# Performance work log

Hardware: AMD Instinct MI355X
Metric: run time of the kernel (lower is better)

Reference implementation:

```python
import jax, jax.numpy as jnp
import numpy as np

N = 65536      # points per cloud
L = 64         # voxel grid side
K_KNN = 16


def _decode(lin):
    x = lin // (L * L); y = (lin // L) % L; z = lin % L
    return np.stack([x, y, z], -1).astype(np.int32)


def _build_nbr(out_c, in_c, r):
    # Minkowski-style kernel map: for each output coord and each of (2r+1)^3
    # offsets, index of matching input coord, sentinel=len(in_c) if absent.
    g = np.arange(-r, r + 1)
    offs = np.stack(np.meshgrid(g, g, g, indexing='ij'), -1).reshape(-1, 3)
    S = 80  # encode side (coords in [-r, L+r) shifted by 8 fit in [0,80))
    def enc(c):
        return ((c[..., 0].astype(np.int64) + 8) * S + (c[..., 1] + 8)) * S + (c[..., 2] + 8)
    kin = enc(in_c)
    order = np.argsort(kin).astype(np.int32)
    skin = kin[order]
    nin = len(in_c)
    rows = []
    for i in range(0, len(out_c), 8192):
        q = out_c[i:i + 8192, None, :] + offs[None]
        kq = enc(q).reshape(-1)
        pos = np.clip(np.searchsorted(skin, kq), 0, nin - 1)
        ok = skin[pos] == kq
        rows.append(np.where(ok, order[pos], nin).astype(np.int32).reshape(-1, len(offs)))
    return np.concatenate(rows, 0)


def _knn(qc, rc, k):
    # brute-force knn (matches pytorch3d.ops.knn_points indices up to order;
    # downstream mean/softmax are permutation invariant)
    q = qc.astype(np.float32); r = rc.astype(np.float32)
    rn = (r * r).sum(1)
    out = []
    for i in range(0, len(q), 4096):
        qb = q[i:i + 4096]
        d = (qb * qb).sum(1)[:, None] + rn[None, :] - 2.0 * qb @ r.T
        out.append(np.argpartition(d, k, axis=1)[:, :k].astype(np.int32))
    return np.concatenate(out, 0)


def setup_inputs():
    rng = np.random.default_rng(0)
    prev_C = _decode(rng.permutation(L ** 3)[:N])
    cur_C = _decode(rng.permutation(L ** 3)[:N])
    nbr_interp = _build_nbr(cur_C, prev_C, 4)  # 9^3 = 729 offsets
    nbr3 = _build_nbr(cur_C, cur_C, 1)         # 3^3 = 27 offsets
    knn_idx = _knn(cur_C, prev_C, K_KNN)
    key = jax.random.key(0)
    ks = jax.random.split(key, 32)
    f32 = jnp.float32
    def w(k, shape, s):
        return jax.random.normal(k, shape, f32) * s
    C = 32
    return dict(
        prev_F=w(ks[0], (N, 1), 1.0),
        prev_C=jnp.asarray(prev_C), cur_C=jnp.asarray(cur_C),
        nbr_interp=jnp.asarray(nbr_interp), nbr3=jnp.asarray(nbr3),
        knn_idx=jnp.asarray(knn_idx),
        W_interp=w(ks[1], (729, 1, 1), 0.05), b_interp=w(ks[2], (1,), 0.05),
        W_conv0=w(ks[3], (27, 2, C), 0.1), b_conv0=w(ks[4], (C,), 0.05),
        W_conv1=w(ks[5], (C, C), 0.1), b_conv1=w(ks[6], (C,), 0.05),
        Wi00=w(ks[7], (C, C // 4), 0.1), bi00=w(ks[8], (C // 4,), 0.05),
        Wi01=w(ks[9], (27, C // 4, C // 4), 0.1), bi01=w(ks[10], (C // 4,), 0.05),
        Wi02=w(ks[11], (C // 4, C // 2), 0.1), bi02=w(ks[12], (C // 2,), 0.05),
        Wi10=w(ks[13], (27, C, C // 4), 0.1), bi10=w(ks[14], (C // 4,), 0.05),
        Wi11=w(ks[15], (27, C // 4, C // 2), 0.1), bi11=w(ks[16], (C // 2,), 0.05),
        Wq=w(ks[17], (1, 1), 0.5), bq=w(ks[18], (1,), 0.1),
        Wk=w(ks[19], (4, 1), 0.5), bk=w(ks[20], (1,), 0.1),
        Wv=w(ks[21], (4, 1), 0.5), bv=w(ks[22], (1,), 0.1),
        Wlin=w(ks[23], (1, 1), 0.5), blin=w(ks[24], (1,), 0.1),
        ln1_g=jnp.ones((1,), f32), ln1_b=jnp.zeros((1,), f32),
        ln2_g=jnp.ones((1,), f32), ln2_b=jnp.zeros((1,), f32),
    )


def _sparse_conv(feats, nbr, W, b):
    # gather-GEMM-scatter sparse conv; sentinel index == len(feats) -> zero row
    fpad = jnp.concatenate([feats, jnp.zeros((1, feats.shape[1]), feats.dtype)], 0)
    g = fpad[nbr]  # [Nout, K, Cin]
    return jnp.einsum('nkc,kcd->nd', g, W) + b


def _ln(x, g, b, eps=1e-5):
    m = jnp.mean(x, -1, keepdims=True)
    v = jnp.var(x, -1, keepdims=True)
    return (x - m) * jax.lax.rsqrt(v + eps) * g + b


def reference(prev_F, prev_C, cur_C, nbr_interp, nbr3, knn_idx,
              W_interp, b_interp, W_conv0, b_conv0, W_conv1, b_conv1,
              Wi00, bi00, Wi01, bi01, Wi02, bi02, Wi10, bi10, Wi11, bi11,
              Wq, bq, Wk, bk, Wv, bv, Wlin, blin, ln1_g, ln1_b, ln2_g, ln2_b):
    # interp: generative 9^3 sparse conv from previous coords onto current coords
    context = _sparse_conv(prev_F, nbr_interp, W_interp, b_interp)  # [N,1]

    # Target_Point_Transformer_Last (channels = in_channels = 1, head=1, k=16)
    pxyz = prev_C.astype(jnp.float32)
    cxyz = cur_C.astype(jnp.float32)
    knn_xyz = pxyz[knn_idx] - cxyz[:, None, :]          # [N,16,3]
    knn_xyz = knn_xyz / jnp.max(knn_xyz)                # global-max normalization
    knn_feat = prev_F[knn_idx]                          # [N,16,1]
    x = jnp.mean(knn_feat, axis=1)                      # init_feature [N,1]
    nf = jnp.concatenate([knn_feat, knn_xyz], axis=2)   # [N,16,4]
    Q = (x @ Wq + bq)[:, None, :]                       # [N,1,1] (head=1)
    Kt = (nf @ Wk + bk)[:, None, :, :]                  # [N,1,16,1]
    V = (nf @ Wv + bv)[:, None, :, :]
    att = jnp.einsum('nhd,nhkd->nhk', Q, Kt) / 1.0      # d = sqrt(channels=1)
    att = jax.nn.softmax(att, axis=-1)
    af = jnp.einsum('nhk,nhkd->nhd', att, V).reshape(-1, 1)
    x1 = x + af
    x1 = _ln(x1, ln1_g, ln1_b)
    x1 = x1 + x1 @ Wlin + blin
    interp_feat = _ln(x1, ln2_g, ln2_b)                 # [N,1]

    ctx = jnp.concatenate([context, interp_feat], axis=-1)  # [N,2]
    h = jax.nn.relu(_sparse_conv(ctx, nbr3, W_conv0, b_conv0))  # [N,32]
    # InceptionResNet
    o = jax.nn.relu(h @ Wi00 + bi00)                         # 1x1 conv [N,8]
    o0 = jax.nn.relu(_sparse_conv(o, nbr3, Wi01, bi01))
    o0 = jax.nn.relu(o0 @ Wi02 + bi02)                       # [N,16]
    o1 = jax.nn.relu(_sparse_conv(h, nbr3, Wi10, bi10))
    o1 = jax.nn.relu(_sparse_conv(o1, nbr3, Wi11, bi11))     # [N,16]
    blk = jnp.concatenate([o0, o1], axis=-1) + h
    out = jax.nn.relu(blk) @ W_conv1 + b_conv1               # 1x1 conv [N,32]
    return out
```

## Files before the change

### kernel.cpp

```cpp
#include <hip/hip_runtime.h>


#define NPTS 65536
#define GD 72
#define GSX (GD*GD)
#define GRID_FLOATS (GD*GD*GD)
#define CD 64
#define CELLS (CD*CD*CD)

__global__ __launch_bounds__(256) void k_scatter(const float* __restrict__ prev_F,
                                                 const int* __restrict__ prev_C,
                                                 const int* __restrict__ cur_C,
                                                 float* __restrict__ gridF,
                                                 int* __restrict__ pidg) {
    int m = blockIdx.x * 256 + threadIdx.x;
    int x = prev_C[m*3+0], y = prev_C[m*3+1], z = prev_C[m*3+2];
    gridF[(x+4)*GSX + (y+4)*GD + (z+4)] = prev_F[m];
    int cx = cur_C[m*3+0], cy = cur_C[m*3+1], cz = cur_C[m*3+2];
    pidg[(cx*CD + cy)*CD + cz] = m;
}

__global__ __launch_bounds__(256) void k_ctx_dense(const float* __restrict__ gridF,
                                                   const int* __restrict__ pidg,
                                                   const float* __restrict__ W_interp,
                                                   const float* __restrict__ b_interp,
                                                   float* __restrict__ ctx) {
    __shared__ float tile[16*16*16];
    int bid = blockIdx.x;
    int bx = (bid >> 6) * 8, by = ((bid >> 3) & 7) * 8, bz = (bid & 7) * 8;
    int t = threadIdx.x;
    #pragma unroll
    for (int rep = 0; rep < 16; ++rep) {
        int i = t + rep*256;
        int a = i >> 8, b = (i >> 4) & 15, c = i & 15;
        tile[i] = gridF[(bx + a)*GSX + (by + b)*GD + (bz + c)];
    }
    __syncthreads();
    int tz = (t & 3) * 2;
    int ty = (t >> 2) & 7;
    int tx = t >> 5;
    float acc0 = 0.f, acc1 = 0.f;
    for (int dx = 0; dx < 9; ++dx) {
        for (int dy = 0; dy < 9; ++dy) {
            const float* row = &tile[((tx + dx)*16 + (ty + dy))*16 + tz];
            float2 r0 = *(const float2*)(row);
            float2 r1 = *(const float2*)(row + 2);
            float2 r2 = *(const float2*)(row + 4);
            float2 r3 = *(const float2*)(row + 6);
            float2 r4 = *(const float2*)(row + 8);
            float v[10] = {r0.x,r0.y,r1.x,r1.y,r2.x,r2.y,r3.x,r3.y,r4.x,r4.y};
            const float* wp = &W_interp[(dx*9 + dy)*9];
            #pragma unroll
            for (int dz = 0; dz < 9; ++dz) {
                float w = wp[dz];
                acc0 = fmaf(v[dz+0], w, acc0);
                acc1 = fmaf(v[dz+1], w, acc1);
            }
        }
    }
    float bi = b_interp[0];
    int cell = ((bx + tx)*CD + (by + ty))*CD + (bz + tz);
    int2 pids = *(const int2*)(pidg + cell);
    if (pids.x >= 0) ctx[pids.x] = acc0 + bi;
    if (pids.y >= 0) ctx[pids.y] = acc1 + bi;
}


__global__ __launch_bounds__(256, 4) void k_conv0(const int* __restrict__ nbr3,
                                                  const float* __restrict__ ctx,
                                                  const float* __restrict__ W_conv0,
                                                  const float* __restrict__ b_conv0,
                                                  const float* __restrict__ Wi00,
                                                  const float* __restrict__ bi00,
                                                  float* __restrict__ h,
                                                  float* __restrict__ o) {
    __shared__ int   ln[64*27];
    __shared__ float part[3][32][64];
    int tid = threadIdx.x;
    int lane = tid & 63, q = tid >> 6;
    int n0 = blockIdx.x * 64;
    for (int i = tid; i < 64*27; i += 256) ln[i] = nbr3[(size_t)n0*27 + i];
    __syncthreads();
    int kbase = __builtin_amdgcn_readfirstlane(q * 7);
    int n = n0 + lane;
    float ac[32];
    #pragma unroll
    for (int d = 0; d < 32; ++d) ac[d] = 0.f;
    #pragma unroll
    for (int j = 0; j < 7; ++j) {
        int k = kbase + j;
        if (k < 27) {
            int idx = ln[lane*27 + k];
            if (idx < NPTS) {
                float cv = ctx[idx];
                const float* wr = &W_conv0[k*64];
                #pragma unroll
                for (int d = 0; d < 32; ++d) ac[d] = fmaf(cv, wr[d], ac[d]);
            }
        }
    }
    if (q > 0) {
        #pragma unroll
        for (int d = 0; d < 32; ++d) part[q-1][d][lane] = ac[d];
    }
    __syncthreads();
    if (q == 0) {
        #pragma unroll
        for (int d = 0; d < 32; ++d)
            ac[d] = fmaxf(ac[d] + b_conv0[d] + part[0][d][lane] + part[1][d][lane] + part[2][d][lane], 0.f);
        float4* hp = (float4*)(h + (size_t)n*32);
        #pragma unroll
        for (int w = 0; w < 8; ++w) hp[w] = make_float4(ac[w*4], ac[w*4+1], ac[w*4+2], ac[w*4+3]);
        float ov[8];
        #pragma unroll
        for (int j = 0; j < 8; ++j) {
            float tt = bi00[j];
            #pragma unroll
            for (int d = 0; d < 32; ++d) tt = fmaf(ac[d], Wi00[d*8 + j], tt);
            ov[j] = fmaxf(tt, 0.f);
        }
        float4* op = (float4*)(o + (size_t)n*8);
        op[0] = make_float4(ov[0], ov[1], ov[2], ov[3]);
        op[1] = make_float4(ov[4], ov[5], ov[6], ov[7]);
    }
}

__global__ __launch_bounds__(256, 4) void k_mid(const int* __restrict__ nbr3,
                                                const float* __restrict__ h,
                                                const float* __restrict__ o,
                                                const float* __restrict__ Wi01,
                                                const float* __restrict__ bi01,
                                                const float* __restrict__ Wi10,
                                                const float* __restrict__ bi10,
                                                float* __restrict__ o0a,
                                                float* __restrict__ o1a) {
    __shared__ int   ln[64*27];
    __shared__ float part[3][16][64];
    int tid = threadIdx.x;
    int lane = tid & 63, q = tid >> 6;
    int n0 = blockIdx.x * 64;
    for (int i = tid; i < 64*27; i += 256) ln[i] = nbr3[(size_t)n0*27 + i];
    __syncthreads();
    int kbase = __builtin_amdgcn_readfirstlane(q * 7);
    int n = n0 + lane;
    float ac[16];
    #pragma unroll
    for (int d = 0; d < 16; ++d) ac[d] = 0.f;
    #pragma unroll
    for (int j = 0; j < 7; ++j) {
        int k = kbase + j;
        if (k < 27) {
            int idx = ln[lane*27 + k];
            if (idx < NPTS) {
                const float4* orow = (const float4*)(o + (size_t)idx*8);
                float4 oa = orow[0], ob = orow[1];
                const float4* hrow = (const float4*)(h + (size_t)idx*32);
                float4 h0 = hrow[0], h1 = hrow[1], h2 = hrow[2], h3 = hrow[3];
                float4 h4 = hrow[4], h5 = hrow[5], h6 = hrow[6], h7 = hrow[7];
                float oc[8] = {oa.x,oa.y,oa.z,oa.w, ob.x,ob.y,ob.z,ob.w};
                const float* w0 = &Wi01[k*64];
                #pragma unroll
                for (int c = 0; c < 8; ++c)
                    #pragma unroll
                    for (int d = 0; d < 8; ++d) ac[d] = fmaf(oc[c], w0[c*8 + d], ac[d]);
                float hc[32] = {h0.x,h0.y,h0.z,h0.w, h1.x,h1.y,h1.z,h1.w,
                                h2.x,h2.y,h2.z,h2.w, h3.x,h3.y,h3.z,h3.w,
                                h4.x,h4.y,h4.z,h4.w, h5.x,h5.y,h5.z,h5.w,
                                h6.x,h6.y,h6.z,h6.w, h7.x,h7.y,h7.z,h7.w};
                const float* w1 = &Wi10[k*256];
                #pragma unroll
                for (int c = 0; c < 32; ++c)
                    #pragma unroll
                    for (int d = 0; d < 8; ++d) ac[8+d] = fmaf(hc[c], w1[c*8 + d], ac[8+d]);
            }
        }
    }
    if (q > 0) {
        #pragma unroll
        for (int d = 0; d < 16; ++d) part[q-1][d][lane] = ac[d];
    }
    __syncthreads();
    if (q == 0) {
        #pragma unroll
        for (int d = 0; d < 8; ++d) {
            ac[d]   = fmaxf(ac[d]   + bi01[d] + part[0][d][lane]   + part[1][d][lane]   + part[2][d][lane],   0.f);
            ac[8+d] = fmaxf(ac[8+d] + bi10[d] + part[0][8+d][lane] + part[1][8+d][lane] + part[2][8+d][lane], 0.f);
        }
        float4* p0 = (float4*)(o0a + (size_t)n*8);
        p0[0] = make_float4(ac[0], ac[1], ac[2],  ac[3]);
        p0[1] = make_float4(ac[4], ac[5], ac[6],  ac[7]);
        float4* p1 = (float4*)(o1a + (size_t)n*8);
        p1[0] = make_float4(ac[8], ac[9], ac[10], ac[11]);
        p1[1] = make_float4(ac[12],ac[13],ac[14], ac[15]);
    }
}

__global__ __launch_bounds__(256, 4) void k_out(const int* __restrict__ nbr3,
                                                const float* __restrict__ h,
                                                const float* __restrict__ o0a,
                                                const float* __restrict__ o1a,
                                                const float* __restrict__ Wi11,
                                                const float* __restrict__ bi11,
                                                const float* __restrict__ Wi02,
                                                const float* __restrict__ bi02,
                                                const float* __restrict__ W_conv1,
                                                const float* __restrict__ b_conv1,
                                                float* __restrict__ out) {
    __shared__ int   ln[64*27];
    __shared__ float part[3][16][64];
    __shared__ float blkb[32][64];
    int tid = threadIdx.x;
    int lane = tid & 63, q = tid >> 6;
    int n0 = blockIdx.x * 64;
    for (int i = tid; i < 64*27; i += 256) ln[i] = nbr3[(size_t)n0*27 + i];
    __syncthreads();
    int kbase = __builtin_amdgcn_readfirstlane(q * 7);
    int n = n0 + lane;
    float ac[16];
    #pragma unroll
    for (int d = 0; d < 16; ++d) ac[d] = 0.f;
    #pragma unroll
    for (int j = 0; j < 7; ++j) {
        int k = kbase + j;
        if (k < 27) {
            int idx = ln[lane*27 + k];
            if (idx < NPTS) {
                const float4* rp = (const float4*)(o1a + (size_t)idx*8);
                float4 ra = rp[0], rb = rp[1];
                float rc[8] = {ra.x,ra.y,ra.z,ra.w, rb.x,rb.y,rb.z,rb.w};
                const float* wr = &Wi11[k*128];
                #pragma unroll
                for (int c = 0; c < 8; ++c)
                    #pragma unroll
                    for (int d = 0; d < 16; ++d) ac[d] = fmaf(rc[c], wr[c*16 + d], ac[d]);
            }
        }
    }
    if (q > 0) {
        #pragma unroll
        for (int d = 0; d < 16; ++d) part[q-1][d][lane] = ac[d];
    }
    __syncthreads();
    if (q == 0) {
        #pragma unroll
        for (int d = 0; d < 16; ++d)
            ac[d] += bi11[d] + part[0][d][lane] + part[1][d][lane] + part[2][d][lane];
        float blk[32];
        const float4* prow = (const float4*)(o0a + (size_t)n*8);
        float4 pa = prow[0], pb = prow[1];
        float pc[8] = {pa.x,pa.y,pa.z,pa.w, pb.x,pb.y,pb.z,pb.w};
        #pragma unroll
        for (int j = 0; j < 16; ++j) {
            float tt = bi02[j];
            #pragma unroll
            for (int c = 0; c < 8; ++c) tt = fmaf(pc[c], Wi02[c*16 + j], tt);
            blk[j] = fmaxf(tt, 0.f);
        }
        #pragma unroll
        for (int j = 0; j < 16; ++j) blk[16+j] = fmaxf(ac[j], 0.f);
        const float4* hrow = (const float4*)(h + (size_t)n*32);
        #pragma unroll
        for (int w = 0; w < 8; ++w) {
            float4 hv = hrow[w];
            blk[w*4+0] += hv.x; blk[w*4+1] += hv.y; blk[w*4+2] += hv.z; blk[w*4+3] += hv.w;
        }
        #pragma unroll
        for (int e = 0; e < 32; ++e) blkb[e][lane] = fmaxf(blk[e], 0.f);
    }
    __syncthreads();
    int q8 = __builtin_amdgcn_readfirstlane(q * 8);
    float oacc[8];
    #pragma unroll
    for (int d = 0; d < 8; ++d) oacc[d] = b_conv1[q8 + d];
    #pragma unroll
    for (int e = 0; e < 32; ++e) {
        float bl = blkb[e][lane];
        #pragma unroll
        for (int d = 0; d < 8; ++d) oacc[d] = fmaf(bl, W_conv1[e*32 + q8 + d], oacc[d]);
    }
    float4* outp = (float4*)(out + (size_t)n*32 + q8);
    outp[0] = make_float4(oacc[0], oacc[1], oacc[2], oacc[3]);
    outp[1] = make_float4(oacc[4], oacc[5], oacc[6], oacc[7]);
}

extern "C" void kernel_launch(void* const* d_in, const int* in_sizes, int n_in,
                              void* d_out, int out_size, void* d_ws, size_t ws_size,
                              hipStream_t stream) {
    (void)in_sizes; (void)n_in; (void)out_size; (void)ws_size;
    const float* prev_F   = (const float*)d_in[0];
    const int*   prev_C   = (const int*)d_in[1];
    const int*   cur_C    = (const int*)d_in[2];
    const int*   nbr3     = (const int*)d_in[4];
    const float* W_interp = (const float*)d_in[6];
    const float* b_interp = (const float*)d_in[7];
    const float* W_conv0  = (const float*)d_in[8];
    const float* b_conv0  = (const float*)d_in[9];
    const float* W_conv1  = (const float*)d_in[10];
    const float* b_conv1  = (const float*)d_in[11];
    const float* Wi00     = (const float*)d_in[12];
    const float* bi00     = (const float*)d_in[13];
    const float* Wi01     = (const float*)d_in[14];
    const float* bi01     = (const float*)d_in[15];
    const float* Wi02     = (const float*)d_in[16];
    const float* bi02     = (const float*)d_in[17];
    const float* Wi10     = (const float*)d_in[18];
    const float* bi10     = (const float*)d_in[19];
    const float* Wi11     = (const float*)d_in[20];
    const float* bi11     = (const float*)d_in[21];

    float* ws    = (float*)d_ws;
    float* gridF = ws;
    int*   pidg  = (int*)(ws + 373248);
    float* ctx   = ws + 635392;
    float* h     = ws + 700928;
    float* o     = ws + 2798080;
    float* o0a   = ws + 3322368;
    float* o1a   = ws + 3846656;
    float* outp  = (float*)d_out;

    hipMemsetAsync(gridF, 0,    GRID_FLOATS*sizeof(float), stream);
    hipMemsetAsync(pidg,  0xFF, CELLS*sizeof(int),         stream);
    k_scatter  <<<NPTS/256, 256, 0, stream>>>(prev_F, prev_C, cur_C, gridF, pidg);
    k_ctx_dense<<<512,      256, 0, stream>>>(gridF, pidg, W_interp, b_interp, ctx);
    k_conv0    <<<NPTS/64,  256, 0, stream>>>(nbr3, ctx, W_conv0, b_conv0, Wi00, bi00, h, o);
    k_mid      <<<NPTS/64,  256, 0, stream>>>(nbr3, h, o, Wi01, bi01, Wi10, bi10, o0a, o1a);
    k_out      <<<NPTS/64,  256, 0, stream>>>(nbr3, h, o0a, o1a, Wi11, bi11, Wi02, bi02, W_conv1, b_conv1, outp);
}
```

Measured before the change: 375.8 us.

## Merge memsets, pad dense-conv LDS tile, and preload neighbor indices

The two workspace memsets become one by storing point ids offset by one, so zero means empty. The shared-memory tile in the dense 9^3 convolution gets a padded row stride of 20 floats to reduce LDS bank conflicts. The three sparse-conv kernels load all seven neighbor indices from LDS into registers before the gather loop, so the loads can be issued early. The memset merge relies on gridF and pidg being contiguous in the workspace (373248 = 72^3), and the padded tile uses more shared memory.

```diff
diff --git a/kernel.cpp b/kernel.cpp
--- a/kernel.cpp
+++ b/kernel.cpp
@@ -7,6 +7,7 @@
 #define GRID_FLOATS (GD*GD*GD)
 #define CD 64
 #define CELLS (CD*CD*CD)
+#define TS 20
 
 __global__ __launch_bounds__(256) void k_scatter(const float* __restrict__ prev_F,
                                                  const int* __restrict__ prev_C,
@@ -17,7 +18,7 @@
     int x = prev_C[m*3+0], y = prev_C[m*3+1], z = prev_C[m*3+2];
     gridF[(x+4)*GSX + (y+4)*GD + (z+4)] = prev_F[m];
     int cx = cur_C[m*3+0], cy = cur_C[m*3+1], cz = cur_C[m*3+2];
-    pidg[(cx*CD + cy)*CD + cz] = m;
+    pidg[(cx*CD + cy)*CD + cz] = m + 1;
 }
 
 __global__ __launch_bounds__(256) void k_ctx_dense(const float* __restrict__ gridF,
@@ -25,7 +26,7 @@
                                                    const float* __restrict__ W_interp,
                                                    const float* __restrict__ b_interp,
                                                    float* __restrict__ ctx) {
-    __shared__ float tile[16*16*16];
+    __shared__ float tile[16*16*TS];
     int bid = blockIdx.x;
     int bx = (bid >> 6) * 8, by = ((bid >> 3) & 7) * 8, bz = (bid & 7) * 8;
     int t = threadIdx.x;
@@ -33,7 +34,7 @@
     for (int rep = 0; rep < 16; ++rep) {
         int i = t + rep*256;
         int a = i >> 8, b = (i >> 4) & 15, c = i & 15;
-        tile[i] = gridF[(bx + a)*GSX + (by + b)*GD + (bz + c)];
+        tile[(a*16 + b)*TS + c] = gridF[(bx + a)*GSX + (by + b)*GD + (bz + c)];
     }
     __syncthreads();
     int tz = (t & 3) * 2;
@@ -42,7 +43,7 @@
     float acc0 = 0.f, acc1 = 0.f;
     for (int dx = 0; dx < 9; ++dx) {
         for (int dy = 0; dy < 9; ++dy) {
-            const float* row = &tile[((tx + dx)*16 + (ty + dy))*16 + tz];
+            const float* row = &tile[((tx + dx)*16 + (ty + dy))*TS + tz];
             float2 r0 = *(const float2*)(row);
             float2 r1 = *(const float2*)(row + 2);
             float2 r2 = *(const float2*)(row + 4);
@@ -61,8 +62,8 @@
     float bi = b_interp[0];
     int cell = ((bx + tx)*CD + (by + ty))*CD + (bz + tz);
     int2 pids = *(const int2*)(pidg + cell);
-    if (pids.x >= 0) ctx[pids.x] = acc0 + bi;
-    if (pids.y >= 0) ctx[pids.y] = acc1 + bi;
+    if (pids.x > 0) ctx[pids.x - 1] = acc0 + bi;
+    if (pids.y > 0) ctx[pids.y - 1] = acc1 + bi;
 }
 
 
@@ -83,6 +84,14 @@
     __syncthreads();
     int kbase = __builtin_amdgcn_readfirstlane(q * 7);
     int n = n0 + lane;
+    int idxs[7];
+    #pragma unroll
+    for (int j = 0; j < 7; ++j) {
+        int k = kbase + j;
+        int kk = (k < 27) ? k : 26;
+        int raw = ln[lane*27 + kk];
+        idxs[j] = (k < 27) ? raw : NPTS;
+    }
     float ac[32];
     #pragma unroll
     for (int d = 0; d < 32; ++d) ac[d] = 0.f;
@@ -90,7 +99,7 @@
     for (int j = 0; j < 7; ++j) {
         int k = kbase + j;
         if (k < 27) {
-            int idx = ln[lane*27 + k];
+            int idx = idxs[j];
             if (idx < NPTS) {
                 float cv = ctx[idx];
                 const float* wr = &W_conv0[k*64];
@@ -143,6 +152,14 @@
     __syncthreads();
     int kbase = __builtin_amdgcn_readfirstlane(q * 7);
     int n = n0 + lane;
+    int idxs[7];
+    #pragma unroll
+    for (int j = 0; j < 7; ++j) {
+        int k = kbase + j;
+        int kk = (k < 27) ? k : 26;
+        int raw = ln[lane*27 + kk];
+        idxs[j] = (k < 27) ? raw : NPTS;
+    }
     float ac[16];
     #pragma unroll
     for (int d = 0; d < 16; ++d) ac[d] = 0.f;
@@ -150,7 +167,7 @@
     for (int j = 0; j < 7; ++j) {
         int k = kbase + j;
         if (k < 27) {
-            int idx = ln[lane*27 + k];
+            int idx = idxs[j];
             if (idx < NPTS) {
                 const float4* orow = (const float4*)(o + (size_t)idx*8);
                 float4 oa = orow[0], ob = orow[1];
@@ -216,6 +233,14 @@
     __syncthreads();
     int kbase = __builtin_amdgcn_readfirstlane(q * 7);
     int n = n0 + lane;
+    int idxs[7];
+    #pragma unroll
+    for (int j = 0; j < 7; ++j) {
+        int k = kbase + j;
+        int kk = (k < 27) ? k : 26;
+        int raw = ln[lane*27 + kk];
+        idxs[j] = (k < 27) ? raw : NPTS;
+    }
     float ac[16];
     #pragma unroll
     for (int d = 0; d < 16; ++d) ac[d] = 0.f;
@@ -223,7 +248,7 @@
     for (int j = 0; j < 7; ++j) {
         int k = kbase + j;
         if (k < 27) {
-            int idx = ln[lane*27 + k];
+            int idx = idxs[j];
             if (idx < NPTS) {
                 const float4* rp = (const float4*)(o1a + (size_t)idx*8);
                 float4 ra = rp[0], rb = rp[1];
@@ -318,8 +343,7 @@
     float* o1a   = ws + 3846656;
     float* outp  = (float*)d_out;
 
-    hipMemsetAsync(gridF, 0,    GRID_FLOATS*sizeof(float), stream);
-    hipMemsetAsync(pidg,  0xFF, CELLS*sizeof(int),         stream);
+    hipMemsetAsync(gridF, 0, (GRID_FLOATS + CELLS)*sizeof(float), stream);
     k_scatter  <<<NPTS/256, 256, 0, stream>>>(prev_F, prev_C, cur_C, gridF, pidg);
     k_ctx_dense<<<512,      256, 0, stream>>>(gridF, pidg, W_interp, b_interp, ctx);
     k_conv0    <<<NPTS/64,  256, 0, stream>>>(nbr3, ctx, W_conv0, b_conv0, Wi00, bi00, h, o);
```

After: 362.8 us. 3.5% less time.
